# Optimization experiments

Hardware: AMD Instinct MI355X
Metric: run time of the kernel (lower is better)

## Reference

```python
import jax, jax.numpy as jnp
import numpy as np

N_MEM = 50000
MATCH_THR2 = 0.01   # squared-distance match threshold (0.1 m)
EMA = 0.5           # EMA factor for matched-descriptor update
EPS = 1e-8


def _bilinear_depth(depth, uv):
    # depth: [H, W]; uv: [M, 2] pixel coords (u = x/col, v = y/row)
    H, W = depth.shape
    u = jnp.clip(uv[:, 0], 0.0, W - 1.001)
    v = jnp.clip(uv[:, 1], 0.0, H - 1.001)
    u0 = jnp.floor(u); v0 = jnp.floor(v)
    du = u - u0; dv = v - v0
    u0i = u0.astype(jnp.int32); v0i = v0.astype(jnp.int32)
    d00 = depth[v0i, u0i]
    d01 = depth[v0i, u0i + 1]
    d10 = depth[v0i + 1, u0i]
    d11 = depth[v0i + 1, u0i + 1]
    return d00 * (1 - du) * (1 - dv) + d01 * du * (1 - dv) + d10 * (1 - du) * dv + d11 * du * dv


def pix2world(points, depth_map, pose, K):
    # points [B,M,2], depth_map [B,1,H,W], pose [B,3,4] cam->world, K [B,3,3]
    d = jax.vmap(_bilinear_depth)(depth_map[:, 0], points)            # [B,M]
    pix = jnp.concatenate([points, jnp.ones_like(points[..., :1])], -1)  # [B,M,3]
    Kinv = jnp.linalg.inv(K)
    cam = jnp.einsum('bij,bmj->bmi', Kinv, pix) * d[..., None]        # [B,M,3]
    world = jnp.einsum('bij,bmj->bmi', pose[:, :, :3], cam) + pose[:, :, 3][:, None, :]
    valid = (d > 0) & jnp.isfinite(world).all(-1)                      # [B,M]
    return world, valid


def memory_write(pts, desc, valid, mem_pts, mem_desc, next_ptr):
    # pts [P,3], desc [P,D]; mem_pts [N,3], mem_desc [N,D]
    d2 = (jnp.sum(pts * pts, -1, keepdims=True)
          - 2.0 * pts @ mem_pts.T
          + jnp.sum(mem_pts * mem_pts, -1)[None, :])                  # [P,N]
    idx = jnp.argmin(d2, axis=1)                                       # [P]
    dmin = jnp.take_along_axis(d2, idx[:, None], axis=1)[:, 0]
    match = (dmin < MATCH_THR2) & valid
    n_match = match.sum()
    # returned descriptors come from the (non-differentiable) memory buffer;
    # unmatched entries return their own descriptor (cos=1 -> zero loss/grad)
    matched_desc = jax.lax.stop_gradient(jnp.where(match[:, None], mem_desc[idx], desc))
    # --- state update (buffers: no gradient) ---
    dsg = jax.lax.stop_gradient(desc)
    psg = jax.lax.stop_gradient(pts)
    unm = (~match) & valid
    slots = (next_ptr + jnp.cumsum(unm.astype(jnp.int32)) - 1) % N_MEM
    widx = jnp.where(unm, slots, idx)                                  # [P]
    old_pts = mem_pts[widx]; old_desc = mem_desc[widx]
    upd = old_desc * EMA + dsg * (1.0 - EMA)
    upd = upd / (jnp.linalg.norm(upd, axis=-1, keepdims=True) + EPS)
    new_desc_vals = jnp.where(match[:, None], upd, jnp.where(unm[:, None], dsg, old_desc))
    new_pts_vals = jnp.where(unm[:, None], psg, old_pts)
    new_mem_desc = mem_desc.at[widx].set(new_desc_vals)
    new_mem_pts = mem_pts.at[widx].set(new_pts_vals)
    return matched_desc, n_match, new_mem_pts, new_mem_desc


def setup_inputs() -> dict:
    key = jax.random.key(0)
    ks = jax.random.split(key, 8)
    B, M, D, H, W = 8, 512, 256, 480, 640
    points = jax.random.uniform(ks[0], (B, M, 2), jnp.float32) * jnp.array([W - 2.0, H - 2.0])
    depth_map = 0.5 + 4.5 * jax.random.uniform(ks[1], (B, 1, H, W), jnp.float32)
    # proper rotations via QR + small translations
    A = np.asarray(jax.random.normal(ks[2], (B, 3, 3)))
    Rs = np.stack([np.linalg.qr(A[b])[0] for b in range(B)]).astype(np.float32)
    t = np.asarray(jax.random.normal(ks[3], (B, 3, 1))) * 2.0
    pose = jnp.asarray(np.concatenate([Rs, t.astype(np.float32)], axis=2))  # [B,3,4]
    Kmat = jnp.broadcast_to(jnp.array([[320.0, 0.0, 320.0], [0.0, 320.0, 240.0], [0.0, 0.0, 1.0]], jnp.float32), (B, 3, 3))
    descriptors = jax.random.normal(ks[4], (B, M, D), jnp.float32)
    mem_pts = (jax.random.uniform(ks[5], (N_MEM, 3), jnp.float32) - 0.5) * 16.0
    mem_desc = jax.random.normal(ks[6], (N_MEM, D), jnp.float32)
    mem_desc = mem_desc / (jnp.linalg.norm(mem_desc, axis=-1, keepdims=True) + EPS)
    return {"points": points, "depth_map": depth_map, "pose": pose, "K": Kmat,
            "descriptors": descriptors, "mem_pts": mem_pts, "mem_desc": mem_desc,
            "next_ptr": 20000}


def reference(points, depth_map, pose, K, descriptors, mem_pts, mem_desc, next_ptr):
    world, valid = pix2world(points, depth_map, pose, K)               # [B,M,3], [B,M]
    P = world.shape[0] * world.shape[1]
    pts = world.reshape(P, 3)
    desc = descriptors.reshape(P, -1)
    vmask = valid.reshape(P)
    pts = jnp.where(vmask[:, None], pts, 1e6)   # invalid points never match
    matched_desc, n_match, new_mem_pts, new_mem_desc = memory_write(
        pts, desc, vmask, mem_pts, mem_desc, next_ptr)
    a = desc / jnp.maximum(jnp.linalg.norm(desc, axis=-1, keepdims=True), EPS)
    b = matched_desc / jnp.maximum(jnp.linalg.norm(matched_desc, axis=-1, keepdims=True), EPS)
    cos = jnp.sum(a * b, -1)                                           # [P]
    nv = jnp.maximum(vmask.sum(), 1)
    loss = 1.0 - jnp.sum(cos * vmask) / nv
    return loss, n_match, new_mem_pts, new_mem_desc
```

## Files before the change

kernel.cpp:

```cpp
#include <hip/hip_runtime.h>
#include <math.h>

#define N_MEM   50000
#define P_TOT   4096
#define DDIM    256
#define HDIM    480
#define WDIM    640
#define CHUNK   391
#define DISTB   1024
#define COPYB   512
#define THR2    0.01f
#define EPSF    1e-8f
typedef unsigned long long ull;

__device__ __forceinline__ unsigned fsort(float x) {
    unsigned b = __float_as_uint(x);
    return (b & 0x80000000u) ? ~b : (b | 0x80000000u);
}

__global__ void k_world(const float* __restrict__ points,
                        const float* __restrict__ depth,
                        const float* __restrict__ pose,
                        const float* __restrict__ Kmat,
                        float4* __restrict__ pts_out,
                        int* __restrict__ flags_out,
                        ull* __restrict__ minkey)
{
    int p = blockIdx.x * 256 + threadIdx.x;
    if (p >= P_TOT) return;
    minkey[p] = 0xFFFFFFFFFFFFFFFFULL;
    int b = p >> 9;
    const float* K = Kmat + b * 9;
    float a00=K[0],a01=K[1],a02=K[2],a10=K[3],a11=K[4],a12=K[5],a20=K[6],a21=K[7],a22=K[8];
    float det = a00*(a11*a22-a12*a21) - a01*(a10*a22-a12*a20) + a02*(a10*a21-a11*a20);
    float id = 1.0f/det;
    float i00=(a11*a22-a12*a21)*id, i01=(a02*a21-a01*a22)*id, i02=(a01*a12-a02*a11)*id;
    float i10=(a12*a20-a10*a22)*id, i11=(a00*a22-a02*a20)*id, i12=(a02*a10-a00*a12)*id;
    float i20=(a10*a21-a11*a20)*id, i21=(a01*a20-a00*a21)*id, i22=(a00*a11-a01*a10)*id;

    float u = points[p*2+0], v = points[p*2+1];
    float uc = fminf(fmaxf(u, 0.f), (float)WDIM - 1.001f);
    float vc = fminf(fmaxf(v, 0.f), (float)HDIM - 1.001f);
    float u0 = floorf(uc), v0 = floorf(vc);
    float du = uc - u0, dv = vc - v0;
    int u0i = (int)u0, v0i = (int)v0;
    const float* dm = depth + (size_t)b * HDIM * WDIM;
    float d00 = dm[v0i*WDIM + u0i];
    float d01 = dm[v0i*WDIM + u0i + 1];
    float d10 = dm[(v0i+1)*WDIM + u0i];
    float d11 = dm[(v0i+1)*WDIM + u0i + 1];
    float d = d00*(1.f-du)*(1.f-dv) + d01*du*(1.f-dv) + d10*(1.f-du)*dv + d11*du*dv;

    float cx = (i00*u + i01*v + i02) * d;
    float cy = (i10*u + i11*v + i12) * d;
    float cz = (i20*u + i21*v + i22) * d;
    const float* T = pose + b * 12;
    float wx = T[0]*cx + T[1]*cy + T[2]*cz  + T[3];
    float wy = T[4]*cx + T[5]*cy + T[6]*cz  + T[7];
    float wz = T[8]*cx + T[9]*cy + T[10]*cz + T[11];
    int val = (d > 0.f) && isfinite(wx) && isfinite(wy) && isfinite(wz);
    float4 o = val ? make_float4(wx, wy, wz, 0.f) : make_float4(1e6f, 1e6f, 1e6f, 0.f);
    pts_out[p] = o;
    flags_out[p] = val;
}

__global__ __launch_bounds__(256) void k_main(const float4* __restrict__ pts,
                                              const float* __restrict__ mem_pts,
                                              const float* __restrict__ mem_desc,
                                              ull* __restrict__ minkey,
                                              float* __restrict__ out_pts,
                                              float* __restrict__ out_desc,
                                              int* __restrict__ winner)
{
    __shared__ float4 sm[CHUNK];
    int bid = blockIdx.x;
    int t = threadIdx.x;
    if (bid < DISTB) {
        int pb = bid >> 7;
        int ch = bid & 127;
        int j0 = ch * CHUNK;
        int cnt = min(CHUNK, N_MEM - j0);
        for (int j = t; j < cnt; j += 256) {
            float mx = mem_pts[(j0 + j) * 3 + 0];
            float my = mem_pts[(j0 + j) * 3 + 1];
            float mz = mem_pts[(j0 + j) * 3 + 2];
            sm[j] = make_float4(mx, my, mz, mx*mx + my*my + mz*mz);
        }
        __syncthreads();
        int p0 = pb * 512 + t;
        float4 P0 = pts[p0], P1 = pts[p0+256];
        float pp0 = P0.x*P0.x + P0.y*P0.y + P0.z*P0.z;
        float pp1 = P1.x*P1.x + P1.y*P1.y + P1.z*P1.z;
        float bd0 = 3.4e38f, bd1 = 3.4e38f;
        int bi0 = 0, bi1 = 0;
        for (int j = 0; j < cnt; ++j) {
            float4 mv = sm[j];
            float dot0 = P0.x*mv.x + P0.y*mv.y + P0.z*mv.z;
            float dot1 = P1.x*mv.x + P1.y*mv.y + P1.z*mv.z;
            float d0 = pp0 - 2.f*dot0 + mv.w;
            float d1 = pp1 - 2.f*dot1 + mv.w;
            if (d0 < bd0) { bd0 = d0; bi0 = j0 + j; }
            if (d1 < bd1) { bd1 = d1; bi1 = j0 + j; }
        }
        ull k0 = ((ull)fsort(bd0) << 32) | (unsigned)bi0;
        ull k1 = ((ull)fsort(bd1) << 32) | (unsigned)bi1;
        atomicMin(&minkey[p0],       k0);
        atomicMin(&minkey[p0 + 256], k1);
    } else {
        const long tid = (long)(bid - DISTB) * 256 + t;
        const long stride = (long)COPYB * 256;
        const float2* ds = (const float2*)mem_desc;
        float2* dd = (float2*)out_desc;
        const long ND2 = (long)N_MEM * DDIM / 2;
        long k = tid * 4;
        const long stride4 = stride * 4;
        for (; k + 3 < ND2; k += stride4) {
            float2 a0 = ds[k+0], a1 = ds[k+1], a2 = ds[k+2], a3 = ds[k+3];
            dd[k+0] = a0; dd[k+1] = a1; dd[k+2] = a2; dd[k+3] = a3;
        }
        for (; k < ND2; ++k) dd[k] = ds[k];
        const float2* ps = (const float2*)mem_pts;
        float2* pd = (float2*)out_pts;
        for (long i = tid; i < (long)N_MEM * 3 / 2; i += stride) pd[i] = ps[i];
        for (long i = tid; i < N_MEM; i += stride) winner[i] = -1;
    }
}

__global__ __launch_bounds__(256) void k_scan(const ull* __restrict__ minkey,
                                              int* __restrict__ flags,
                                              int* __restrict__ idx_ws,
                                              const int* __restrict__ next_ptr,
                                              int* __restrict__ widx,
                                              int* __restrict__ winner,
                                              float* __restrict__ dout)
{
    __shared__ int su[256];
    __shared__ int smc[256];
    int t = threadIdx.x;
    int base = t * 16;
    const ull thr_key = ((ull)fsort(THR2)) << 32;
    int um[16], iv[16];
    int usum = 0, msum = 0;
    for (int k = 0; k < 16; k++) {
        ull key = minkey[base + k];
        int v = flags[base + k] & 1;
        int m = (key < thr_key) && v;
        int u = (!m) && v;
        iv[k] = (int)(key & 0xffffffffULL);
        um[k] = u; usum += u; msum += m;
        flags[base + k] = v | (m << 1) | (u << 2);
    }
    su[t] = usum; smc[t] = msum;
    __syncthreads();
    for (int off = 1; off < 256; off <<= 1) {
        int a = su[t], b = (t >= off) ? su[t - off] : 0;
        int c = smc[t], d = (t >= off) ? smc[t - off] : 0;
        __syncthreads();
        su[t] = a + b; smc[t] = c + d;
        __syncthreads();
    }
    int excl = su[t] - usum;
    int np_ = *next_ptr;
    int run = excl;
    for (int k = 0; k < 16; k++) {
        int wv;
        if (um[k]) { run += 1; wv = (np_ + run - 1) % N_MEM; }
        else       { wv = iv[k]; }
        widx[base + k] = wv;
        idx_ws[base + k] = iv[k];
        atomicMax(&winner[wv], base + k);
    }
    if (t == 255) dout[1] = (float)smc[255];
}

__global__ __launch_bounds__(256) void k_scatloss(const int* __restrict__ widx,
                                                  const int* __restrict__ flags,
                                                  const int* __restrict__ winner,
                                                  const float* __restrict__ desc,
                                                  const float4* __restrict__ pts,
                                                  const float* __restrict__ mem_pts,
                                                  const float* __restrict__ mem_desc,
                                                  float* __restrict__ out_pts,
                                                  float* __restrict__ out_desc,
                                                  float* __restrict__ cos_ws)
{
    __shared__ float red[16];
    int p = blockIdx.x;
    int t = threadIdx.x;
    int f = flags[p];
    int v = f & 1, m = (f >> 1) & 1, u = (f >> 2) & 1;
    int wi = widx[p];
    int win = (winner[wi] == p);
    if (!m && !win) {
        if (t == 0) cos_ws[p] = v ? 1.f : 0.f;
        return;
    }
    float dsg = desc[p * DDIM + t];
    float old = mem_desc[(long)wi * DDIM + t];
    float val, cosv;
    if (m) {
        float up = old * 0.5f + dsg * 0.5f;
        float sdd = dsg * dsg, smm2 = old * old, sdm = dsg * old, suu = up * up;
        for (int off = 32; off; off >>= 1) {
            sdd  += __shfl_xor(sdd,  off);
            smm2 += __shfl_xor(smm2, off);
            sdm  += __shfl_xor(sdm,  off);
            suu  += __shfl_xor(suu,  off);
        }
        int w = t >> 6;
        if ((t & 63) == 0) { red[w] = sdd; red[4+w] = smm2; red[8+w] = sdm; red[12+w] = suu; }
        __syncthreads();
        float dd  = red[0] + red[1] + red[2] + red[3];
        float mm2 = red[4] + red[5] + red[6] + red[7];
        float dm  = red[8] + red[9] + red[10] + red[11];
        float uu  = red[12] + red[13] + red[14] + red[15];
        cosv = dm / (fmaxf(sqrtf(dd), EPSF) * fmaxf(sqrtf(mm2), EPSF));
        val = up / (sqrtf(uu) + EPSF);
    } else {
        cosv = v ? 1.f : 0.f;
        val = u ? dsg : old;
    }
    if (win) {
        out_desc[(long)wi * DDIM + t] = val;
        if (t == 0) {
            float px, py, pz;
            if (u) { float4 P = pts[p]; px = P.x; py = P.y; pz = P.z; }
            else   { px = mem_pts[wi*3]; py = mem_pts[wi*3+1]; pz = mem_pts[wi*3+2]; }
            out_pts[wi*3+0] = px; out_pts[wi*3+1] = py; out_pts[wi*3+2] = pz;
        }
    }
    if (t == 0) cos_ws[p] = cosv;
}

__global__ __launch_bounds__(256) void k_final(const float* __restrict__ cos_ws,
                                               const int* __restrict__ flags,
                                               float* __restrict__ dout)
{
    __shared__ float ss[256];
    __shared__ float sv[256];
    int t = threadIdx.x;
    float s = 0.f, v = 0.f;
    for (int k = t; k < P_TOT; k += 256) {
        s += cos_ws[k];
        v += (float)(flags[k] & 1);
    }
    ss[t] = s; sv[t] = v;
    __syncthreads();
    for (int off = 128; off; off >>= 1) {
        if (t < off) { ss[t] += ss[t + off]; sv[t] += sv[t + off]; }
        __syncthreads();
    }
    if (t == 0) {
        float nv = fmaxf(sv[0], 1.f);
        dout[0] = 1.f - ss[0] / nv;
    }
}

extern "C" void kernel_launch(void* const* d_in, const int* in_sizes, int n_in,
                              void* d_out, int out_size, void* d_ws, size_t ws_size,
                              hipStream_t stream)
{
    const float* points   = (const float*)d_in[0];
    const float* depth    = (const float*)d_in[1];
    const float* pose     = (const float*)d_in[2];
    const float* Kmat     = (const float*)d_in[3];
    const float* desc     = (const float*)d_in[4];
    const float* mem_pts  = (const float*)d_in[5];
    const float* mem_desc = (const float*)d_in[6];
    const int*   next_ptr = (const int*)d_in[7];

    float* out      = (float*)d_out;
    float* out_pts  = out + 2;
    float* out_desc = out + 2 + (long)N_MEM * 3;

    char* ws = (char*)d_ws;
    float4* pts_ws  = (float4*)(ws);
    int* flags_ws   = (int*)(ws + 65536);
    int* idx_ws     = (int*)(ws + 81920);
    int* widx_ws    = (int*)(ws + 98304);
    int* winner_ws  = (int*)(ws + 114688);
    float* cos_ws   = (float*)(ws + 314688);
    ull* minkey_ws  = (ull*)(ws + 331072);

    k_world   <<<16, 256, 0, stream>>>(points, depth, pose, Kmat, pts_ws, flags_ws, minkey_ws);
    k_main    <<<DISTB + COPYB, 256, 0, stream>>>(pts_ws, mem_pts, mem_desc, minkey_ws,
                                                  out_pts, out_desc, winner_ws);
    k_scan    <<<1, 256, 0, stream>>>(minkey_ws, flags_ws, idx_ws, next_ptr,
                                      widx_ws, winner_ws, out);
    k_scatloss<<<P_TOT, 256, 0, stream>>>(widx_ws, flags_ws, winner_ws, desc, pts_ws,
                                          mem_pts, mem_desc, out_pts, out_desc, cos_ws);
    k_final   <<<1, 256, 0, stream>>>(cos_ws, flags_ws, out);
}
```

Before: 180.2 us.

## Register-tile four points per thread and reset winner slots only where written

```diff
diff --git a/kernel.cpp b/kernel.cpp
--- a/kernel.cpp
+++ b/kernel.cpp
@@ -6,7 +6,7 @@
 #define DDIM    256
 #define HDIM    480
 #define WDIM    640
-#define CHUNK   391
+#define CHUNK   196
 #define DISTB   1024
 #define COPYB   512
 #define THR2    0.01f
@@ -69,43 +69,50 @@
                                               const float* __restrict__ mem_desc,
                                               ull* __restrict__ minkey,
                                               float* __restrict__ out_pts,
-                                              float* __restrict__ out_desc,
-                                              int* __restrict__ winner)
+                                              float* __restrict__ out_desc)
 {
     __shared__ float4 sm[CHUNK];
     int bid = blockIdx.x;
     int t = threadIdx.x;
     if (bid < DISTB) {
-        int pb = bid >> 7;
-        int ch = bid & 127;
+        int pb = bid >> 8;
+        int ch = bid & 255;
         int j0 = ch * CHUNK;
         int cnt = min(CHUNK, N_MEM - j0);
-        for (int j = t; j < cnt; j += 256) {
-            float mx = mem_pts[(j0 + j) * 3 + 0];
-            float my = mem_pts[(j0 + j) * 3 + 1];
-            float mz = mem_pts[(j0 + j) * 3 + 2];
-            sm[j] = make_float4(mx, my, mz, mx*mx + my*my + mz*mz);
-        }
-        __syncthreads();
-        int p0 = pb * 512 + t;
-        float4 P0 = pts[p0], P1 = pts[p0+256];
+        if (t < cnt) {
+            float mx = mem_pts[(j0 + t) * 3 + 0];
+            float my = mem_pts[(j0 + t) * 3 + 1];
+            float mz = mem_pts[(j0 + t) * 3 + 2];
+            sm[t] = make_float4(mx, my, mz, mx*mx + my*my + mz*mz);
+        }
+        __syncthreads();
+        int p0 = pb * 1024 + t;
+        float4 P0 = pts[p0], P1 = pts[p0+256], P2 = pts[p0+512], P3 = pts[p0+768];
         float pp0 = P0.x*P0.x + P0.y*P0.y + P0.z*P0.z;
         float pp1 = P1.x*P1.x + P1.y*P1.y + P1.z*P1.z;
-        float bd0 = 3.4e38f, bd1 = 3.4e38f;
-        int bi0 = 0, bi1 = 0;
+        float pp2 = P2.x*P2.x + P2.y*P2.y + P2.z*P2.z;
+        float pp3 = P3.x*P3.x + P3.y*P3.y + P3.z*P3.z;
+        float bd0 = 3.4e38f, bd1 = 3.4e38f, bd2 = 3.4e38f, bd3 = 3.4e38f;
+        int bi0 = 0, bi1 = 0, bi2 = 0, bi3 = 0;
         for (int j = 0; j < cnt; ++j) {
             float4 mv = sm[j];
             float dot0 = P0.x*mv.x + P0.y*mv.y + P0.z*mv.z;
             float dot1 = P1.x*mv.x + P1.y*mv.y + P1.z*mv.z;
+            float dot2 = P2.x*mv.x + P2.y*mv.y + P2.z*mv.z;
+            float dot3 = P3.x*mv.x + P3.y*mv.y + P3.z*mv.z;
             float d0 = pp0 - 2.f*dot0 + mv.w;
             float d1 = pp1 - 2.f*dot1 + mv.w;
+            float d2 = pp2 - 2.f*dot2 + mv.w;
+            float d3 = pp3 - 2.f*dot3 + mv.w;
             if (d0 < bd0) { bd0 = d0; bi0 = j0 + j; }
             if (d1 < bd1) { bd1 = d1; bi1 = j0 + j; }
-        }
-        ull k0 = ((ull)fsort(bd0) << 32) | (unsigned)bi0;
-        ull k1 = ((ull)fsort(bd1) << 32) | (unsigned)bi1;
-        atomicMin(&minkey[p0],       k0);
-        atomicMin(&minkey[p0 + 256], k1);
+            if (d2 < bd2) { bd2 = d2; bi2 = j0 + j; }
+            if (d3 < bd3) { bd3 = d3; bi3 = j0 + j; }
+        }
+        atomicMin(&minkey[p0],       ((ull)fsort(bd0) << 32) | (unsigned)bi0);
+        atomicMin(&minkey[p0 + 256], ((ull)fsort(bd1) << 32) | (unsigned)bi1);
+        atomicMin(&minkey[p0 + 512], ((ull)fsort(bd2) << 32) | (unsigned)bi2);
+        atomicMin(&minkey[p0 + 768], ((ull)fsort(bd3) << 32) | (unsigned)bi3);
     } else {
         const long tid = (long)(bid - DISTB) * 256 + t;
         const long stride = (long)COPYB * 256;
@@ -122,13 +129,11 @@
         const float2* ps = (const float2*)mem_pts;
         float2* pd = (float2*)out_pts;
         for (long i = tid; i < (long)N_MEM * 3 / 2; i += stride) pd[i] = ps[i];
-        for (long i = tid; i < N_MEM; i += stride) winner[i] = -1;
     }
 }
 
 __global__ __launch_bounds__(256) void k_scan(const ull* __restrict__ minkey,
                                               int* __restrict__ flags,
-                                              int* __restrict__ idx_ws,
                                               const int* __restrict__ next_ptr,
                                               int* __restrict__ widx,
                                               int* __restrict__ winner,
@@ -139,7 +144,7 @@
     int t = threadIdx.x;
     int base = t * 16;
     const ull thr_key = ((ull)fsort(THR2)) << 32;
-    int um[16], iv[16];
+    int um[16], iv[16], wvv[16];
     int usum = 0, msum = 0;
     for (int k = 0; k < 16; k++) {
         ull key = minkey[base + k];
@@ -167,9 +172,12 @@
         if (um[k]) { run += 1; wv = (np_ + run - 1) % N_MEM; }
         else       { wv = iv[k]; }
         widx[base + k] = wv;
-        idx_ws[base + k] = iv[k];
-        atomicMax(&winner[wv], base + k);
-    }
+        wvv[k] = wv;
+        winner[wv] = -1;
+    }
+    __syncthreads();
+    for (int k = 0; k < 16; k++)
+        atomicMax(&winner[wvv[k]], base + k);
     if (t == 255) dout[1] = (float)smc[255];
 }
 
@@ -276,16 +284,15 @@
     char* ws = (char*)d_ws;
     float4* pts_ws  = (float4*)(ws);
     int* flags_ws   = (int*)(ws + 65536);
-    int* idx_ws     = (int*)(ws + 81920);
-    int* widx_ws    = (int*)(ws + 98304);
-    int* winner_ws  = (int*)(ws + 114688);
-    float* cos_ws   = (float*)(ws + 314688);
-    ull* minkey_ws  = (ull*)(ws + 331072);
+    int* widx_ws    = (int*)(ws + 81920);
+    int* winner_ws  = (int*)(ws + 98304);
+    float* cos_ws   = (float*)(ws + 298304);
+    ull* minkey_ws  = (ull*)(ws + 314688);
 
     k_world   <<<16, 256, 0, stream>>>(points, depth, pose, Kmat, pts_ws, flags_ws, minkey_ws);
     k_main    <<<DISTB + COPYB, 256, 0, stream>>>(pts_ws, mem_pts, mem_desc, minkey_ws,
-                                                  out_pts, out_desc, winner_ws);
-    k_scan    <<<1, 256, 0, stream>>>(minkey_ws, flags_ws, idx_ws, next_ptr,
+                                                  out_pts, out_desc);
+    k_scan    <<<1, 256, 0, stream>>>(minkey_ws, flags_ws, next_ptr,
                                       widx_ws, winner_ws, out);
     k_scatloss<<<P_TOT, 256, 0, stream>>>(widx_ws, flags_ws, winner_ws, desc, pts_ws,
                                           mem_pts, mem_desc, out_pts, out_desc, cos_ws);
```

After: 177.0 us. About the same (-1.8%).
